# Kernel optimization log

Hardware: AMD Instinct MI355X
Metric: run time of the kernel (lower is better)

## Reference

```python
import jax, jax.numpy as jnp
import numpy as np

B, FH, FW, T = 128, 26, 26, 50
A, NUM_CLASSES = 5, 20
IGNORE_THRESH = 0.75
COORD_SCALE, NOOBJ_SCALE, OBJ_SCALE, CLASS_SCALE = 1.0, 1.0, 5.0, 1.0
ANCHORS = jnp.array([[1.3221, 1.73145], [3.19275, 4.00944], [5.05587, 8.09892],
                     [9.47112, 4.84053], [11.2364, 10.0071]], dtype=jnp.float32)


def xywh2xxyy(b):
    return jnp.stack([b[:, 0] - b[:, 2] / 2, b[:, 1] - b[:, 3] / 2,
                      b[:, 0] + b[:, 2] / 2, b[:, 1] + b[:, 3] / 2], axis=1)


def xxyy2xywh(b):
    return jnp.stack([(b[:, 0] + b[:, 2]) / 2, (b[:, 1] + b[:, 3]) / 2,
                      b[:, 2] - b[:, 0], b[:, 3] - b[:, 1]], axis=1)


def pair_iou(b1, b2):
    # b1: [N,4] xxyy, b2: [K,4] xxyy -> [N,K]
    xi1 = jnp.maximum(b1[:, None, 0], b2[None, :, 0])
    yi1 = jnp.maximum(b1[:, None, 1], b2[None, :, 1])
    xi2 = jnp.minimum(b1[:, None, 2], b2[None, :, 2])
    yi2 = jnp.minimum(b1[:, None, 3], b2[None, :, 3])
    inter = jnp.maximum(xi2 - xi1, 0.0) * jnp.maximum(yi2 - yi1, 0.0)
    a1 = ((b1[:, 2] - b1[:, 0]) * (b1[:, 3] - b1[:, 1]))[:, None]
    a2 = ((b2[:, 2] - b2[:, 0]) * (b2[:, 3] - b2[:, 1]))[None, :]
    return inter / (a1 + a2 - inter)


def make_all_anchors(F_H, F_W):
    ys, xs = jnp.meshgrid(jnp.arange(F_H), jnp.arange(F_W), indexing='ij')
    cells = jnp.stack([xs.ravel(), ys.ravel()], axis=-1).astype(jnp.float32)  # [K,2] (c_x, c_y)
    K = F_H * F_W
    all_anch = jnp.concatenate([jnp.broadcast_to(cells[:, None, :], (K, A, 2)),
                                jnp.broadcast_to(ANCHORS[None, :, :], (K, A, 2))], axis=-1)
    return all_anch.reshape(K * A, 4)  # (c_x, c_y, p_w, p_h), top-left-cell coords


def _build_target_single(box_deltas, gt, all_anch, anch_xxyy, F_H, F_W):
    # box_deltas: [K*A,4] (sig tx, sig ty, exp tw, exp th); gt: [T,5]
    K = F_H * F_W
    valid = gt[:, :4].sum(-1) > 0
    scale = jnp.array([F_W, F_H, F_W, F_H], dtype=jnp.float32)
    gt_xxyy = gt[:, :4] * scale  # [T,4] grid units
    # predicted boxes
    pred = jnp.stack([all_anch[:, 0] + box_deltas[:, 0], all_anch[:, 1] + box_deltas[:, 1],
                      all_anch[:, 2] * box_deltas[:, 2], all_anch[:, 3] * box_deltas[:, 3]], axis=1)
    pred_xxyy = xywh2xxyy(pred)
    ious = pair_iou(pred_xxyy, gt_xxyy)                       # [K*A, T]
    ious = jnp.where(valid[None, :], ious, -1.0)
    max_iou = ious.max(axis=-1)                               # [K*A]
    pos_any = jnp.any(max_iou > IGNORE_THRESH)
    iou_mask0 = jnp.where(pos_any & (max_iou >= IGNORE_THRESH), 0.0, NOOBJ_SCALE).reshape(K, A)
    # anchor-gt overlaps for responsibility assignment
    overlaps = pair_iou(anch_xxyy, gt_xxyy).reshape(K, A, T)
    gt_xcycwh = xxyy2xywh(gt_xxyy)                            # [T,4]
    cx = jnp.clip(jnp.floor(gt_xcycwh[:, 0]).astype(jnp.int32), 0, F_W - 1)
    cy = jnp.clip(jnp.floor(gt_xcycwh[:, 1]).astype(jnp.int32), 0, F_H - 1)
    cell = cy * F_W + cx                                      # [T]
    aidx = jnp.argmax(overlaps[cell, :, jnp.arange(T)], axis=-1)  # [T]
    anch_ka = all_anch.reshape(K, A, 4)
    assigned = anch_ka[cell, aidx]                            # [T,4]
    tgt_box = jnp.stack([gt_xcycwh[:, 0] - assigned[:, 0], gt_xcycwh[:, 1] - assigned[:, 1],
                         gt_xcycwh[:, 2] / assigned[:, 2], gt_xcycwh[:, 3] / assigned[:, 3]], axis=1)
    miou_t = max_iou.reshape(K, A)[cell, aidx]                # [T]
    cls_t = gt[:, 4]
    carry0 = (jnp.zeros((K, A)), iou_mask0, jnp.zeros((K, A, 4)),
              jnp.zeros((K, A)), jnp.zeros((K, A)), jnp.zeros((K, A)))
    def step(c, xs):
        it, im, bt, bm, ct, cm = c
        ce, an, v, tb, cl, mi = xs
        def w(arr, new):
            return arr.at[ce, an].set(jnp.where(v, new, arr[ce, an]))
        return (w(it, mi), w(im, OBJ_SCALE), w(bt, tb), w(bm, 1.0), w(ct, cl), w(cm, 1.0)), None
    (it, im, bt, bm, ct, cm), _ = jax.lax.scan(step, carry0, (cell, aidx, valid, tgt_box, cls_t, miou_t))
    return it, im, bt, bm, ct, cm


def setup_inputs() -> dict:
    key = jax.random.key(0)
    k1, k2, k3, k4, k5 = jax.random.split(key, 5)
    outputs = jax.random.normal(k1, (B, A * (5 + NUM_CLASSES), FH, FW), dtype=jnp.float32) * 0.1
    x1 = jax.random.uniform(k2, (B, T, 1), minval=0.02, maxval=0.75)
    y1 = jax.random.uniform(k3, (B, T, 1), minval=0.02, maxval=0.75)
    wh = jax.random.uniform(k4, (B, T, 2), minval=0.05, maxval=0.2)
    cls = jax.random.randint(k5, (B, T, 1), 0, NUM_CLASSES).astype(jnp.float32)
    targets = jnp.concatenate([x1, y1, x1 + wh[..., :1], y1 + wh[..., 1:]], axis=-1)
    targets = jnp.concatenate([targets, cls], axis=-1)  # [B, T, 5]
    return {"outputs": outputs, "targets": targets}


def reference(outputs, targets):
    Bn, _, F_H, F_W = outputs.shape
    out = outputs.transpose(0, 2, 3, 1).reshape(Bn, F_H * F_W * A, 5 + NUM_CLASSES)
    xy = jax.nn.sigmoid(out[..., 0:2])
    wh = jnp.exp(out[..., 2:4])
    conf = jax.nn.sigmoid(out[..., 4])            # [B, K*A]
    cls_score = out[..., 5:]                      # [B, K*A, C]
    box_delta = jnp.concatenate([xy, wh], axis=-1)  # [B, K*A, 4]
    all_anch = make_all_anchors(F_H, F_W)
    anch_xcycwh = all_anch.at[:, :2].add(0.5)
    anch_xxyy = xywh2xxyy(anch_xcycwh)
    it, im, bt, bm, ct, cm = jax.vmap(
        lambda d, g: _build_target_single(d, g, all_anch, anch_xxyy, F_H, F_W))(box_delta, targets)
    it = it.reshape(Bn, -1)
    im = im.reshape(Bn, -1)
    bt = bt.reshape(Bn, -1, 4)
    bm = bm.reshape(Bn, -1, 1)
    ct = ct.reshape(Bn, -1).astype(jnp.int32)
    cm = cm.reshape(Bn, -1)
    box_loss = COORD_SCALE * jnp.sum((box_delta * bm - bt * bm) ** 2) / 2.0 / Bn
    iou_loss = jnp.sum((conf * im - it * im) ** 2) / 2.0 / Bn
    logp = jax.nn.log_softmax(cls_score, axis=-1)
    ce = -jnp.take_along_axis(logp, ct[..., None], axis=-1)[..., 0]
    class_loss = CLASS_SCALE * jnp.sum(cm * ce) / Bn
    return box_loss + iou_loss + class_loss
```

## Files before the change

### kernel.cpp

```cpp
#include <hip/hip_runtime.h>
#include <math.h>

constexpr int BN = 128;
constexpr int FH = 26, FW = 26;
constexpr int T  = 50;
constexpr int A  = 5;
constexpr int NC = 20;
constexpr int K  = FH * FW;
constexpr int KA = K * A;
constexpr int CH = A * (5 + NC);

constexpr float IGNORE_THRESH = 0.75f;
constexpr float OBJ_SCALE = 5.0f;

constexpr int GCH   = (KA + 255) / 256;
constexpr int NPART = BN * GCH;

__constant__ float ANCW[A] = {1.3221f, 3.19275f, 5.05587f, 9.47112f, 11.2364f};
__constant__ float ANCH[A] = {1.73145f, 4.00944f, 8.09892f, 4.84053f, 10.0071f};

__device__ __forceinline__ float fast_sigmoid(float x) {
    return __builtin_amdgcn_rcpf(1.0f + __expf(-x));
}

__global__ __launch_bounds__(256) void yolo_main(
        const float* __restrict__ outputs,
        const float* __restrict__ targets,
        float* __restrict__ Lp, float* __restrict__ Mp, int* __restrict__ Anyp) {
    __shared__ float4 sbox[T];
    __shared__ float4 stb[T];
    __shared__ float  scls[T];
    __shared__ int    wtab[256];
    __shared__ float  redl[4], redm[4];
    __shared__ int    reda[4];

    const int b    = blockIdx.y;
    const int tid  = threadIdx.x;
    const int base = blockIdx.x * 256;
    const int s    = base + tid;
    const bool live = s < KA;

    const int a = live ? (s / K) : 0;
    const int k = live ? (s - a * K) : 0;
    const float* ob = outputs + (size_t)b * CH * K + (size_t)(a * 25) * K;
    float o0 = 0, o1 = 0, o2 = 0, o3 = 0, o4 = 0;
    if (live) {
        o0 = ob[0 * K + k];
        o1 = ob[1 * K + k];
        o2 = ob[2 * K + k];
        o3 = ob[3 * K + k];
        o4 = ob[4 * K + k];
    }

    wtab[tid] = -1;
    int myslot = -1;
    if (tid < T) {
        const float* gt = targets + ((size_t)b * T + tid) * 5;
        float rx1 = gt[0], ry1 = gt[1], rx2 = gt[2], ry2 = gt[3];
        bool valid = (rx1 + ry1 + rx2 + ry2) > 0.0f;
        float x1 = rx1 * FW, y1 = ry1 * FH, x2 = rx2 * FW, y2 = ry2 * FH;
        float w = x2 - x1, h = y2 - y1;

        float cxf = 0.5f * (x1 + x2), cyf = 0.5f * (y1 + y2);
        int cx = (int)floorf(cxf); cx = min(max(cx, 0), FW - 1);
        int cy = (int)floorf(cyf); cy = min(max(cy, 0), FH - 1);
        int cell = cy * FW + cx;

        float acx = (float)cx + 0.5f, acy = (float)cy + 0.5f;
        float best = -1.0f; int ai = 0;
        for (int aa = 0; aa < A; ++aa) {
            float aw = ANCW[aa], ah = ANCH[aa];
            float xi1 = fmaxf(acx - 0.5f * aw, x1), yi1 = fmaxf(acy - 0.5f * ah, y1);
            float xi2 = fminf(acx + 0.5f * aw, x2), yi2 = fminf(acy + 0.5f * ah, y2);
            float inter = fmaxf(xi2 - xi1, 0.0f) * fmaxf(yi2 - yi1, 0.0f);
            float iou = inter / (aw * ah + w * h - inter);
            if (iou > best) { best = iou; ai = aa; }
        }

        sbox[tid] = valid ? make_float4(x1, y1, x2, y2)
                          : make_float4(1e18f, 1e18f, -1e18f, -1e18f);
        stb[tid]  = make_float4(cxf - (float)cx, cyf - (float)cy,
                                w / ANCW[ai], h / ANCH[ai]);
        scls[tid] = gt[4];
        if (valid) myslot = ai * K + cell;
    }
    __syncthreads();

    if (myslot >= 0) {
        int local = myslot - base;
        if ((unsigned)local < 256u) atomicMax(&wtab[local], tid);
    }
    __syncthreads();

    float loss = 0.0f, masked = 0.0f;
    int anyf = 0;

    if (live) {
        const int yy = k / FW, xx = k - yy * FW;
        float s0 = fast_sigmoid(o0), s1 = fast_sigmoid(o1);
        float e2 = __expf(o2),       e3 = __expf(o3);
        float px = (float)xx + s0, py = (float)yy + s1;
        float pw = ANCW[a] * e2,  ph = ANCH[a] * e3;
        float px1 = px - 0.5f * pw, px2 = px + 0.5f * pw;
        float py1 = py - 0.5f * ph, py2 = py + 0.5f * ph;
        float parea = pw * ph;

        float m = -1.0f;
        #pragma unroll 10
        for (int t = 0; t < T; ++t) {
            float4 bx = sbox[t];
            float garea = (bx.z - bx.x) * (bx.w - bx.y);
            float xi1 = fmaxf(px1, bx.x), yi1 = fmaxf(py1, bx.y);
            float xi2 = fminf(px2, bx.z), yi2 = fminf(py2, bx.w);
            float iw = fmaxf(xi2 - xi1, 0.0f), ih = fmaxf(yi2 - yi1, 0.0f);
            float inter = iw * ih;
            float iou = inter * __builtin_amdgcn_rcpf(parea + garea - inter);
            m = fmaxf(m, iou);
        }
        anyf = (m > IGNORE_THRESH) ? 1 : 0;

        float conf = fast_sigmoid(o4);
        int w = wtab[tid];
        if (w >= 0) {
            float d = (conf - m) * OBJ_SCALE;
            loss += 0.5f * d * d;
            float4 tb = stb[w];
            float d0 = s0 - tb.x, d1 = s1 - tb.y;
            float d2 = e2 - tb.z, d3 = e3 - tb.w;
            loss += 0.5f * (d0 * d0 + d1 * d1 + d2 * d2 + d3 * d3);

            float v[NC];
            #pragma unroll
            for (int c = 0; c < NC; ++c) v[c] = ob[(5 + c) * K + k];
            float mx = v[0];
            #pragma unroll
            for (int c = 1; c < NC; ++c) mx = fmaxf(mx, v[c]);
            float se = 0.0f;
            #pragma unroll
            for (int c = 0; c < NC; ++c) se += __expf(v[c] - mx);
            int cls = (int)scls[w];
            loss += (__logf(se) + mx) - v[cls];
        } else {
            float term = 0.5f * conf * conf;
            loss += term;
            if (m >= IGNORE_THRESH) masked += term;
        }
    }

    for (int off = 32; off > 0; off >>= 1) {
        loss   += __shfl_down(loss, off);
        masked += __shfl_down(masked, off);
    }
    anyf = __any(anyf) ? 1 : 0;
    int lane = tid & 63, wv = tid >> 6;
    if (lane == 0) { redl[wv] = loss; redm[wv] = masked; reda[wv] = anyf; }
    __syncthreads();
    if (tid == 0) {
        int idx = b * GCH + blockIdx.x;
        Lp[idx]   = redl[0] + redl[1] + redl[2] + redl[3];
        Mp[idx]   = redm[0] + redm[1] + redm[2] + redm[3];
        Anyp[idx] = reda[0] | reda[1] | reda[2] | reda[3];
    }
}

__global__ __launch_bounds__(128) void yolo_fix(
        const float* __restrict__ Lp, const float* __restrict__ Mp,
        const int* __restrict__ Anyp, float* __restrict__ out) {
    __shared__ float red[2];
    int tid = threadIdx.x;
    float L = 0.0f, M = 0.0f;
    int any = 0;
    if (tid < BN) {
        #pragma unroll
        for (int c = 0; c < GCH; ++c) {
            int idx = tid * GCH + c;
            L += Lp[idx];
            M += Mp[idx];
            any |= Anyp[idx];
        }
    }
    float acc = L - (any ? M : 0.0f);
    for (int off = 32; off > 0; off >>= 1) acc += __shfl_down(acc, off);
    if ((tid & 63) == 0) red[tid >> 6] = acc;
    __syncthreads();
    if (tid == 0) out[0] = (red[0] + red[1]) * (1.0f / (float)BN);
}

extern "C" void kernel_launch(void* const* d_in, const int* in_sizes, int n_in,
                              void* d_out, int out_size, void* d_ws, size_t ws_size,
                              hipStream_t stream) {
    const float* outputs = (const float*)d_in[0];
    const float* targets = (const float*)d_in[1];
    float* out = (float*)d_out;

    float* Lp   = (float*)d_ws;
    float* Mp   = Lp + NPART;
    int*   Anyp = (int*)(Mp + NPART);

    yolo_main<<<dim3(GCH, BN), 256, 0, stream>>>(outputs, targets, Lp, Mp, Anyp);
    yolo_fix<<<1, 128, 0, stream>>>(Lp, Mp, Anyp, out);
}
```

Measured before the change: 92.06 us.

## Fuse final reduction into main kernel via last-block atomic counter

Removes the separate single-block reduction kernel. Each block now bumps a global atomic counter after writing its partials, and the last block to finish does the final sum, so the second launch is replaced by a memset of the counter. Target-box preprocessing is also spread across the four waves (t_own = lane*4 + wave) so all waves share that work. The cost is a threadfence and an atomic per block, plus a memset node.

```diff
diff --git a/kernel.cpp b/kernel.cpp
--- a/kernel.cpp
+++ b/kernel.cpp
@@ -13,8 +13,8 @@
 constexpr float IGNORE_THRESH = 0.75f;
 constexpr float OBJ_SCALE = 5.0f;
 
-constexpr int GCH   = (KA + 255) / 256;
-constexpr int NPART = BN * GCH;
+constexpr int GCH  = (KA + 255) / 256;
+constexpr int NBLK = BN * GCH;
 
 __constant__ float ANCW[A] = {1.3221f, 3.19275f, 5.05587f, 9.47112f, 11.2364f};
 __constant__ float ANCH[A] = {1.73145f, 4.00944f, 8.09892f, 4.84053f, 10.0071f};
@@ -26,13 +26,15 @@
 __global__ __launch_bounds__(256) void yolo_main(
         const float* __restrict__ outputs,
         const float* __restrict__ targets,
-        float* __restrict__ Lp, float* __restrict__ Mp, int* __restrict__ Anyp) {
+        float* __restrict__ Lp, float* __restrict__ Mp, int* __restrict__ Anyp,
+        unsigned* __restrict__ cnt, float* __restrict__ out) {
     __shared__ float4 sbox[T];
     __shared__ float4 stb[T];
     __shared__ float  scls[T];
     __shared__ int    wtab[256];
     __shared__ float  redl[4], redm[4];
     __shared__ int    reda[4];
+    __shared__ int    lastFlag;
 
     const int b    = blockIdx.y;
     const int tid  = threadIdx.x;
@@ -53,9 +55,11 @@
     }
 
     wtab[tid] = -1;
+    const int lane = tid & 63, wv = tid >> 6;
+    const int t_own = lane * 4 + wv;
     int myslot = -1;
-    if (tid < T) {
-        const float* gt = targets + ((size_t)b * T + tid) * 5;
+    if (t_own < T) {
+        const float* gt = targets + ((size_t)b * T + t_own) * 5;
         float rx1 = gt[0], ry1 = gt[1], rx2 = gt[2], ry2 = gt[3];
         bool valid = (rx1 + ry1 + rx2 + ry2) > 0.0f;
         float x1 = rx1 * FW, y1 = ry1 * FH, x2 = rx2 * FW, y2 = ry2 * FH;
@@ -77,18 +81,18 @@
             if (iou > best) { best = iou; ai = aa; }
         }
 
-        sbox[tid] = valid ? make_float4(x1, y1, x2, y2)
-                          : make_float4(1e18f, 1e18f, -1e18f, -1e18f);
-        stb[tid]  = make_float4(cxf - (float)cx, cyf - (float)cy,
-                                w / ANCW[ai], h / ANCH[ai]);
-        scls[tid] = gt[4];
+        sbox[t_own] = valid ? make_float4(x1, y1, x2, y2)
+                            : make_float4(1e18f, 1e18f, -1e18f, -1e18f);
+        stb[t_own]  = make_float4(cxf - (float)cx, cyf - (float)cy,
+                                  w / ANCW[ai], h / ANCH[ai]);
+        scls[t_own] = gt[4];
         if (valid) myslot = ai * K + cell;
     }
     __syncthreads();
 
     if (myslot >= 0) {
         int local = myslot - base;
-        if ((unsigned)local < 256u) atomicMax(&wtab[local], tid);
+        if ((unsigned)local < 256u) atomicMax(&wtab[local], t_own);
     }
     __syncthreads();
 
@@ -152,7 +156,6 @@
         masked += __shfl_down(masked, off);
     }
     anyf = __any(anyf) ? 1 : 0;
-    int lane = tid & 63, wv = tid >> 6;
     if (lane == 0) { redl[wv] = loss; redm[wv] = masked; reda[wv] = anyf; }
     __syncthreads();
     if (tid == 0) {
@@ -160,30 +163,33 @@
         Lp[idx]   = redl[0] + redl[1] + redl[2] + redl[3];
         Mp[idx]   = redm[0] + redm[1] + redm[2] + redm[3];
         Anyp[idx] = reda[0] | reda[1] | reda[2] | reda[3];
-    }
-}
-
-__global__ __launch_bounds__(128) void yolo_fix(
-        const float* __restrict__ Lp, const float* __restrict__ Mp,
-        const int* __restrict__ Anyp, float* __restrict__ out) {
-    __shared__ float red[2];
-    int tid = threadIdx.x;
-    float L = 0.0f, M = 0.0f;
-    int any = 0;
-    if (tid < BN) {
-        #pragma unroll
-        for (int c = 0; c < GCH; ++c) {
-            int idx = tid * GCH + c;
-            L += Lp[idx];
-            M += Mp[idx];
-            any |= Anyp[idx];
-        }
-    }
-    float acc = L - (any ? M : 0.0f);
-    for (int off = 32; off > 0; off >>= 1) acc += __shfl_down(acc, off);
-    if ((tid & 63) == 0) red[tid >> 6] = acc;
-    __syncthreads();
-    if (tid == 0) out[0] = (red[0] + red[1]) * (1.0f / (float)BN);
+        __threadfence();
+        unsigned old = atomicAdd(cnt, 1u);
+        lastFlag = (old == (unsigned)(NBLK - 1));
+    }
+    __syncthreads();
+
+    if (lastFlag) {
+        __threadfence();
+        float acc = 0.0f;
+        if (tid < BN) {
+            float L = 0.0f, M = 0.0f;
+            int any = 0;
+            #pragma unroll
+            for (int c = 0; c < GCH; ++c) {
+                int idx = tid * GCH + c;
+                L += Lp[idx];
+                M += Mp[idx];
+                any |= Anyp[idx];
+            }
+            acc = L - (any ? M : 0.0f);
+        }
+        for (int off = 32; off > 0; off >>= 1) acc += __shfl_down(acc, off);
+        if (lane == 0) redl[wv] = acc;
+        __syncthreads();
+        if (tid == 0)
+            out[0] = (redl[0] + redl[1]) * (1.0f / (float)BN);
+    }
 }
 
 extern "C" void kernel_launch(void* const* d_in, const int* in_sizes, int n_in,
@@ -193,10 +199,12 @@
     const float* targets = (const float*)d_in[1];
     float* out = (float*)d_out;
 
-    float* Lp   = (float*)d_ws;
-    float* Mp   = Lp + NPART;
-    int*   Anyp = (int*)(Mp + NPART);
-
-    yolo_main<<<dim3(GCH, BN), 256, 0, stream>>>(outputs, targets, Lp, Mp, Anyp);
-    yolo_fix<<<1, 128, 0, stream>>>(Lp, Mp, Anyp, out);
+    float*    Lp   = (float*)d_ws;
+    float*    Mp   = Lp + NBLK;
+    int*      Anyp = (int*)(Mp + NBLK);
+    unsigned* cnt  = (unsigned*)(Anyp + NBLK);
+
+    hipMemsetAsync(cnt, 0, sizeof(unsigned), stream);
+    yolo_main<<<dim3(GCH, BN), 256, 0, stream>>>(outputs, targets,
+                                                 Lp, Mp, Anyp, cnt, out);
 }
```

Result: slower. 129.0 us (+40.1%).
